# Optimization experiments

Measured on AMD Instinct MI355X. Metric: run time of the kernel, lower is better.

The kernel has to match this reference:

```python
import jax, jax.numpy as jnp
import numpy as np


def setup_inputs() -> dict:
    key = jax.random.key(0)
    ks = jax.random.split(key, 8)
    B, IN, H, OUT = 8192, 1024, 2048, 1024
    SIGMA_MIN, SIGMA_MAX, PHASE = 0.9, 0.999, 2.0 * np.pi
    # recurrence decay params, initialized as in the torch module
    rng = np.random.RandomState(0)
    u1 = rng.random_sample(H)
    u2 = rng.random_sample(H)
    v = -0.5 * np.log(u1 * (SIGMA_MAX ** 2 - SIGMA_MIN ** 2) + SIGMA_MIN ** 2)
    theta = u2 * PHASE
    scale_b = 1.0 / np.sqrt(IN)
    scale_c = 1.0 / np.sqrt(H)
    return {
        "x": jax.random.normal(ks[0], (B, IN), dtype=jnp.float32),
        "h_prev": jax.random.normal(ks[1], (B, H), dtype=jnp.float32),
        "Br": jax.random.normal(ks[2], (H, IN), dtype=jnp.float32) * scale_b,
        "Bi": jax.random.normal(ks[3], (H, IN), dtype=jnp.float32) * scale_b,
        "Cr": jax.random.normal(ks[4], (OUT, H), dtype=jnp.float32) * scale_c,
        "Ci": jax.random.normal(ks[5], (OUT, H), dtype=jnp.float32) * scale_c,
        "v_log": jnp.asarray(np.log(v), dtype=jnp.float32),
        "theta_log": jnp.asarray(np.log(theta), dtype=jnp.float32),
    }


def reference(x, h_prev, Br, Bi, Cr, Ci, v_log, theta_log):
    # effective diagonal recurrence weight w = exp(-exp(v_log) + i*exp(theta_log))
    mag = jnp.exp(-jnp.exp(v_log))            # [H]
    ang = jnp.exp(theta_log)                  # [H]
    wr = mag * jnp.cos(ang)
    wi = mag * jnp.sin(ang)
    # h = B(x) + h_prev * w  (h_prev is real -> imag part comes only from wi)
    # complexLinear on real x: real = x@Br^T, imag = x@Bi^T
    hr = jnp.einsum('bi,hi->bh', x, Br) + h_prev * wr   # [B,H]
    hi = jnp.einsum('bi,hi->bh', x, Bi) + h_prev * wi   # [B,H]
    # out = Re(C(h)) = hr@Cr^T - hi@Ci^T
    out = jnp.einsum('bh,oh->bo', hr, Cr) - jnp.einsum('bh,oh->bo', hi, Ci)
    return out
```

## Files before the change

kernel.cpp:

```cpp
#include <hip/hip_runtime.h>
#include <stdint.h>

typedef unsigned short u16;
typedef short bf16x8 __attribute__((ext_vector_type(8)));
typedef float f32x4 __attribute__((ext_vector_type(4)));

typedef void as1_void __attribute__((address_space(1)));
typedef void as3_void __attribute__((address_space(3)));

__device__ inline u16 f32_to_bf16(float f) {
    uint32_t u = __builtin_bit_cast(uint32_t, f);
    u += 0x7fffu + ((u >> 16) & 1u);
    return (u16)(u >> 16);
}

__device__ inline void gld_lds16(const void* g, void* l) {
    __builtin_amdgcn_global_load_lds((as1_void*)g, (as3_void*)l, 16, 0, 0);
}



__global__ void prep_kernel(const float* __restrict__ Cr, const float* __restrict__ Ci,
                            const float* __restrict__ Br, const float* __restrict__ Bi,
                            const float* __restrict__ v_log, const float* __restrict__ th_log,
                            u16* __restrict__ Ccat, u16* __restrict__ Bcat,
                            u16* __restrict__ Cwbf)
{
    __shared__ float t[32][33];
    const int b = blockIdx.x, tid = threadIdx.x;

    if (b < 2048) {
        int i = b * 256 + tid;
        int e = i * 4;
        int o = e >> 11;
        int h = e & 2047;
        float4 cr = *(const float4*)(Cr + (size_t)o * 2048 + h);
        float4 ci = *(const float4*)(Ci + (size_t)o * 2048 + h);
        ushort4 ucr, uci, ucw;
        ucr.x = f32_to_bf16(cr.x); ucr.y = f32_to_bf16(cr.y);
        ucr.z = f32_to_bf16(cr.z); ucr.w = f32_to_bf16(cr.w);
        uci.x = f32_to_bf16(-ci.x); uci.y = f32_to_bf16(-ci.y);
        uci.z = f32_to_bf16(-ci.z); uci.w = f32_to_bf16(-ci.w);
        float4 vl = *(const float4*)(v_log + h);
        float4 tl = *(const float4*)(th_log + h);
        float mag, ang, wr, wi;
        mag = expf(-expf(vl.x)); ang = expf(tl.x); wr = mag * cosf(ang); wi = mag * sinf(ang);
        ucw.x = f32_to_bf16(cr.x * wr - ci.x * wi);
        mag = expf(-expf(vl.y)); ang = expf(tl.y); wr = mag * cosf(ang); wi = mag * sinf(ang);
        ucw.y = f32_to_bf16(cr.y * wr - ci.y * wi);
        mag = expf(-expf(vl.z)); ang = expf(tl.z); wr = mag * cosf(ang); wi = mag * sinf(ang);
        ucw.z = f32_to_bf16(cr.z * wr - ci.z * wi);
        mag = expf(-expf(vl.w)); ang = expf(tl.w); wr = mag * cosf(ang); wi = mag * sinf(ang);
        ucw.w = f32_to_bf16(cr.w * wr - ci.w * wi);
        *(ushort4*)(Ccat + (size_t)o * 4096 + h)        = ucr;
        *(ushort4*)(Ccat + (size_t)o * 4096 + 2048 + h) = uci;
        *(ushort4*)(Cwbf + (size_t)o * 2048 + h)        = ucw;
    } else {
        int b2 = b - 2048;
        const float* src = (b2 & 2048) ? Bi : Br;
        int colOff = (b2 & 2048) ? 2048 : 0;
        int c0 = (b2 & 31) * 32, r0 = ((b2 >> 5) & 63) * 32;
        int tx = tid & 31, ty = tid >> 5;
#pragma unroll
        for (int j = 0; j < 4; j++)
            t[ty + j * 8][tx] = src[(size_t)(r0 + ty + j * 8) * 1024 + c0 + tx];
        __syncthreads();
#pragma unroll
        for (int j = 0; j < 4; j++)
            Bcat[(size_t)(c0 + ty + j * 8) * 4096 + colOff + r0 + tx] =
                f32_to_bf16(t[tx][ty + j * 8]);
    }
}


__global__ __launch_bounds__(256)
void gemm_splitk_kernel(const u16* __restrict__ A, const u16* __restrict__ B,
                        float* __restrict__ partials)
{
    __shared__ __align__(16) u16 ldsA[128 * 64];
    __shared__ __align__(16) u16 ldsB[128 * 64];
    const int K = 4096;

    const int tid = threadIdx.x, wid = tid >> 6, lane = tid & 63;
    const int quad = lane >> 4, l16 = lane & 15;
    const int wm = wid >> 1, wn = wid & 1;
    const int bm = blockIdx.y, bn = blockIdx.x, bz = blockIdx.z;
    const int kb = bz * 1024;

    const u16* gA[4]; const u16* gB[4];
    u16 *lA[4], *lB[4];
#pragma unroll
    for (int t = 0; t < 4; t++) {
        int s = wid * 256 + t * 64 + lane;
        int sr = s >> 3;
        int sj = (s & 7) ^ (sr & 7);
        lA[t] = ldsA + s * 8;
        lB[t] = ldsB + s * 8;
        gA[t] = A + (size_t)(bm * 128 + sr) * K + sj * 8 + kb;
        gB[t] = B + (size_t)(bn * 128 + sr) * K + sj * 8 + kb;
    }

    const f32x4 fz = {0.f, 0.f, 0.f, 0.f};
    f32x4 acc[4][4];
#pragma unroll
    for (int i = 0; i < 4; i++)
#pragma unroll
        for (int j = 0; j < 4; j++) acc[i][j] = fz;

    for (int k0 = 0; k0 < 1024; k0 += 64) {
        __syncthreads();
#pragma unroll
        for (int t = 0; t < 4; t++) {
            gld_lds16(gA[t] + k0, lA[t]);
            gld_lds16(gB[t] + k0, lB[t]);
        }
        __syncthreads();
#pragma unroll
        for (int ks = 0; ks < 2; ks++) {
            bf16x8 af[4], bfr[4];
#pragma unroll
            for (int i = 0; i < 4; i++) {
                int r = wm * 64 + i * 16 + l16;
                af[i] = *(const bf16x8*)(ldsA + (r * 8 + ((ks * 4 + quad) ^ (r & 7))) * 8);
            }
#pragma unroll
            for (int j = 0; j < 4; j++) {
                int r = wn * 64 + j * 16 + l16;
                bfr[j] = *(const bf16x8*)(ldsB + (r * 8 + ((ks * 4 + quad) ^ (r & 7))) * 8);
            }
#pragma unroll
            for (int i = 0; i < 4; i++)
#pragma unroll
                for (int j = 0; j < 4; j++)
                    acc[i][j] = __builtin_amdgcn_mfma_f32_16x16x32_bf16(af[i], bfr[j], acc[i][j], 0, 0, 0);
        }
    }

    float* P = partials + ((size_t)bz << 20);
    const int gm = bm * 128 + wm * 64, gn = bn * 128 + wn * 64;
#pragma unroll
    for (int i = 0; i < 4; i++)
#pragma unroll
        for (int j = 0; j < 4; j++) {
            int col = gn + j * 16 + l16;
#pragma unroll
            for (int r = 0; r < 4; r++)
                P[(size_t)(gm + i * 16 + quad * 4 + r) * 1024 + col] = acc[i][j][r];
        }
}


__global__ void reduce_cast_kernel(const float* __restrict__ partials,
                                   const float* __restrict__ x,
                                   const float* __restrict__ h_prev,
                                   u16* __restrict__ Wmain,
                                   u16* __restrict__ x_bf,
                                   u16* __restrict__ hp_bf)
{
    const int b = blockIdx.x, tid = threadIdx.x;
    if (b < 1024) {
        int i = b * 256 + tid;
        int e = i * 4;
        float4 s = *(const float4*)(partials + e);
#pragma unroll
        for (int z = 1; z < 4; z++) {
            float4 p = *(const float4*)(partials + ((size_t)z << 20) + e);
            s.x += p.x; s.y += p.y; s.z += p.z; s.w += p.w;
        }
        ushort4 u;
        u.x = f32_to_bf16(s.x); u.y = f32_to_bf16(s.y);
        u.z = f32_to_bf16(s.z); u.w = f32_to_bf16(s.w);
        ((ushort4*)Wmain)[i] = u;
    } else if (b < 9216) {
        int i = (b - 1024) * 256 + tid;
        float4 f = ((const float4*)x)[i];
        ushort4 o;
        o.x = f32_to_bf16(f.x); o.y = f32_to_bf16(f.y);
        o.z = f32_to_bf16(f.z); o.w = f32_to_bf16(f.w);
        ((ushort4*)x_bf)[i] = o;
    } else {
        int i = (b - 9216) * 256 + tid;
        float4 f = ((const float4*)h_prev)[i];
        ushort4 o;
        o.x = f32_to_bf16(f.x); o.y = f32_to_bf16(f.y);
        o.z = f32_to_bf16(f.z); o.w = f32_to_bf16(f.w);
        ((ushort4*)hp_bf)[i] = o;
    }
}


__global__ void reduce_only_kernel(const float* __restrict__ partials,
                                   u16* __restrict__ Wmain) {
    int i = blockIdx.x * blockDim.x + threadIdx.x;
    int e = i * 4;
    float4 s = *(const float4*)(partials + e);
#pragma unroll
    for (int z = 1; z < 4; z++) {
        float4 p = *(const float4*)(partials + ((size_t)z << 20) + e);
        s.x += p.x; s.y += p.y; s.z += p.z; s.w += p.w;
    }
    ushort4 u;
    u.x = f32_to_bf16(s.x); u.y = f32_to_bf16(s.y);
    u.z = f32_to_bf16(s.z); u.w = f32_to_bf16(s.w);
    ((ushort4*)Wmain)[i] = u;
}

__global__ void cast_both_kernel(const float* __restrict__ x,
                                 const float* __restrict__ h_prev,
                                 u16* __restrict__ dst) {
    const int n4x = 8192 * 1024 / 4;
    int i = blockIdx.x * blockDim.x + threadIdx.x;
    float4 f = (i < n4x) ? ((const float4*)x)[i] : ((const float4*)h_prev)[i - n4x];
    ushort4 o;
    o.x = f32_to_bf16(f.x); o.y = f32_to_bf16(f.y);
    o.z = f32_to_bf16(f.z); o.w = f32_to_bf16(f.w);
    ((ushort4*)dst)[i] = o;
}


__global__ __launch_bounds__(512)
void gemm_main_kernel(const u16* __restrict__ Axb, const u16* __restrict__ Ahb,
                      const u16* __restrict__ Bw,  const u16* __restrict__ Bcw,
                      float* __restrict__ out)
{
    __shared__ __align__(16) u16 lds[3][24576];

    const int tid = threadIdx.x, wid = tid >> 6, lane = tid & 63;
    const int quad = lane >> 4, l16 = lane & 15;
    const int wm = wid >> 1, wn = wid & 1;
    const int id = blockIdx.x;
    const int bm = id & 31, bn = id >> 5;

    int srA[4], sjA[4], srB[2], sjB[2];
#pragma unroll
    for (int q = 0; q < 4; q++) {
        int s = q * 512 + tid;
        srA[q] = s >> 3;
        sjA[q] = (s & 7) ^ (srA[q] & 7);
    }
#pragma unroll
    for (int q = 0; q < 2; q++) {
        int s = q * 512 + tid;
        srB[q] = s >> 3;
        sjB[q] = (s & 7) ^ (srB[q] & 7);
    }

    u16* buf0 = &lds[0][0];
    u16* buf1 = &lds[1][0];
    u16* buf2 = &lds[2][0];

    const f32x4 fz = {0.f, 0.f, 0.f, 0.f};
    f32x4 acc[4][4];
#pragma unroll
    for (int i = 0; i < 4; i++)
#pragma unroll
        for (int j = 0; j < 4; j++) acc[i][j] = fz;

    auto stage = [&](int tt, u16* buf) {
        const u16* Ab; const u16* Bb; int KS, koff;
        if (tt < 16) { Ab = Axb; Bb = Bw;  KS = 1024; koff = tt * 64; }
        else         { Ab = Ahb; Bb = Bcw; KS = 2048; koff = (tt - 16) * 64; }
#pragma unroll
        for (int q = 0; q < 4; q++)
            gld_lds16(Ab + (size_t)(bm * 256 + srA[q]) * KS + koff + sjA[q] * 8,
                      buf + (q * 512 + tid) * 8);
#pragma unroll
        for (int q = 0; q < 2; q++)
            gld_lds16(Bb + (size_t)(bn * 128 + srB[q]) * KS + koff + sjB[q] * 8,
                      buf + 16384 + (q * 512 + tid) * 8);
    };

    auto compute = [&](const u16* buf) {
#pragma unroll
        for (int ks = 0; ks < 2; ks++) {
            bf16x8 af[4], bfr[4];
#pragma unroll
            for (int i = 0; i < 4; i++) {
                int r = wm * 64 + i * 16 + l16;
                af[i] = *(const bf16x8*)(buf + (r * 8 + ((ks * 4 + quad) ^ (r & 7))) * 8);
            }
#pragma unroll
            for (int j = 0; j < 4; j++) {
                int r = wn * 64 + j * 16 + l16;
                bfr[j] = *(const bf16x8*)(buf + 16384 + (r * 8 + ((ks * 4 + quad) ^ (r & 7))) * 8);
            }
            __builtin_amdgcn_s_setprio(1);
#pragma unroll
            for (int i = 0; i < 4; i++)
#pragma unroll
                for (int j = 0; j < 4; j++)
                    acc[i][j] = __builtin_amdgcn_mfma_f32_16x16x32_bf16(af[i], bfr[j], acc[i][j], 0, 0, 0);
            __builtin_amdgcn_s_setprio(0);
        }
    };

#define PUBLISH(N)                                          \
    asm volatile("s_waitcnt vmcnt(" #N ")" ::: "memory");   \
    __builtin_amdgcn_s_barrier();                           \
    asm volatile("" ::: "memory")

    stage(0, buf0);
    stage(1, buf1);
    PUBLISH(6);

#pragma unroll 1
    for (int it = 0; it < 15; it++) {
        stage(3 * it + 2, buf2); compute(buf0); PUBLISH(6);
        stage(3 * it + 3, buf0); compute(buf1); PUBLISH(6);
        stage(3 * it + 4, buf1); compute(buf2); PUBLISH(6);
    }
    stage(47, buf2); compute(buf0); PUBLISH(6);
    compute(buf1); PUBLISH(0);
    compute(buf2);
#undef PUBLISH

    const int gm = bm * 256 + wm * 64, gn = bn * 128 + wn * 64;
#pragma unroll
    for (int i = 0; i < 4; i++)
#pragma unroll
        for (int j = 0; j < 4; j++) {
            int col = gn + j * 16 + l16;
#pragma unroll
            for (int r = 0; r < 4; r++)
                out[(size_t)(gm + i * 16 + quad * 4 + r) * 1024 + col] = acc[i][j][r];
        }
}


extern "C" void kernel_launch(void* const* d_in, const int* in_sizes, int n_in,
                              void* d_out, int out_size, void* d_ws, size_t ws_size,
                              hipStream_t stream)
{
    const float* x      = (const float*)d_in[0];
    const float* h_prev = (const float*)d_in[1];
    const float* Br     = (const float*)d_in[2];
    const float* Bi     = (const float*)d_in[3];
    const float* Cr     = (const float*)d_in[4];
    const float* Ci     = (const float*)d_in[5];
    const float* v_log  = (const float*)d_in[6];
    const float* th_log = (const float*)d_in[7];
    float* out = (float*)d_out;

    const size_t MB = 1024 * 1024;
    if (ws_size < 54 * MB) return;
    const bool big = (ws_size >= 86 * MB);

    char* ws = (char*)d_ws;
    u16*   Ccat     = (u16*)ws;
    u16*   Bcat     = (u16*)(ws + 8 * MB);
    float* partials = (float*)(ws + 16 * MB);
    u16*   x_bf     = (u16*)ws;
    u16*   Wmain    = (u16*)(ws + 48 * MB);
    u16*   Cwbf     = (u16*)(ws + 50 * MB);
    u16*   hp_bf    = big ? (u16*)(ws + 54 * MB) : (u16*)(ws + 16 * MB);

    prep_kernel<<<6144, 256, 0, stream>>>(Cr, Ci, Br, Bi, v_log, th_log,
                                          Ccat, Bcat, Cwbf);
    gemm_splitk_kernel<<<dim3(8, 8, 4), 256, 0, stream>>>(Ccat, Bcat, partials);
    if (big) {
        reduce_cast_kernel<<<25600, 256, 0, stream>>>(partials, x, h_prev,
                                                      Wmain, x_bf, hp_bf);
    } else {
        reduce_only_kernel<<<1024, 256, 0, stream>>>(partials, Wmain);
        cast_both_kernel<<<24576, 256, 0, stream>>>(x, h_prev, x_bf);
    }
    gemm_main_kernel<<<256, 512, 0, stream>>>(x_bf, hp_bf, Wmain, Cwbf, out);
}
```

Baseline: 242.2 us.

## Triple-buffer LDS in split-K GEMM to overlap global loads with MFMA

Replaces the single-buffered load-sync-compute loop with a three-stage LDS ring where tile k+2 is fetched via global_load_lds while tile k is computed. Barriers now wait only on vmcnt for the older stage. This hides global memory latency behind MFMA work. It also raises MFMA wave priority with s_setprio. LDS use rises to 96KB per block, which may lower occupancy.

```diff
diff --git a/kernel.cpp b/kernel.cpp
--- a/kernel.cpp
+++ b/kernel.cpp
@@ -77,8 +77,7 @@
 void gemm_splitk_kernel(const u16* __restrict__ A, const u16* __restrict__ B,
                         float* __restrict__ partials)
 {
-    __shared__ __align__(16) u16 ldsA[128 * 64];
-    __shared__ __align__(16) u16 ldsB[128 * 64];
+    __shared__ __align__(16) u16 lds[3][16384];
     const int K = 4096;
 
     const int tid = threadIdx.x, wid = tid >> 6, lane = tid & 63;
@@ -87,18 +86,17 @@
     const int bm = blockIdx.y, bn = blockIdx.x, bz = blockIdx.z;
     const int kb = bz * 1024;
 
-    const u16* gA[4]; const u16* gB[4];
-    u16 *lA[4], *lB[4];
-#pragma unroll
-    for (int t = 0; t < 4; t++) {
-        int s = wid * 256 + t * 64 + lane;
-        int sr = s >> 3;
-        int sj = (s & 7) ^ (sr & 7);
-        lA[t] = ldsA + s * 8;
-        lB[t] = ldsB + s * 8;
-        gA[t] = A + (size_t)(bm * 128 + sr) * K + sj * 8 + kb;
-        gB[t] = B + (size_t)(bn * 128 + sr) * K + sj * 8 + kb;
-    }
+    int sr[4], sj[4];
+#pragma unroll
+    for (int q = 0; q < 4; q++) {
+        int s = q * 256 + tid;
+        sr[q] = s >> 3;
+        sj[q] = (s & 7) ^ (sr[q] & 7);
+    }
+
+    u16* buf0 = &lds[0][0];
+    u16* buf1 = &lds[1][0];
+    u16* buf2 = &lds[2][0];
 
     const f32x4 fz = {0.f, 0.f, 0.f, 0.f};
     f32x4 acc[4][4];
@@ -107,34 +105,61 @@
 #pragma unroll
         for (int j = 0; j < 4; j++) acc[i][j] = fz;
 
-    for (int k0 = 0; k0 < 1024; k0 += 64) {
-        __syncthreads();
-#pragma unroll
-        for (int t = 0; t < 4; t++) {
-            gld_lds16(gA[t] + k0, lA[t]);
-            gld_lds16(gB[t] + k0, lB[t]);
-        }
-        __syncthreads();
+    auto stage = [&](int tt, u16* buf) {
+        int koff = kb + tt * 64;
+#pragma unroll
+        for (int q = 0; q < 4; q++) {
+            gld_lds16(A + (size_t)(bm * 128 + sr[q]) * K + koff + sj[q] * 8,
+                      buf + (q * 256 + tid) * 8);
+            gld_lds16(B + (size_t)(bn * 128 + sr[q]) * K + koff + sj[q] * 8,
+                      buf + 8192 + (q * 256 + tid) * 8);
+        }
+    };
+
+    auto compute = [&](const u16* buf) {
 #pragma unroll
         for (int ks = 0; ks < 2; ks++) {
             bf16x8 af[4], bfr[4];
 #pragma unroll
             for (int i = 0; i < 4; i++) {
                 int r = wm * 64 + i * 16 + l16;
-                af[i] = *(const bf16x8*)(ldsA + (r * 8 + ((ks * 4 + quad) ^ (r & 7))) * 8);
+                af[i] = *(const bf16x8*)(buf + (r * 8 + ((ks * 4 + quad) ^ (r & 7))) * 8);
             }
 #pragma unroll
             for (int j = 0; j < 4; j++) {
                 int r = wn * 64 + j * 16 + l16;
-                bfr[j] = *(const bf16x8*)(ldsB + (r * 8 + ((ks * 4 + quad) ^ (r & 7))) * 8);
+                bfr[j] = *(const bf16x8*)(buf + 8192 + (r * 8 + ((ks * 4 + quad) ^ (r & 7))) * 8);
             }
+            __builtin_amdgcn_s_setprio(1);
 #pragma unroll
             for (int i = 0; i < 4; i++)
 #pragma unroll
                 for (int j = 0; j < 4; j++)
                     acc[i][j] = __builtin_amdgcn_mfma_f32_16x16x32_bf16(af[i], bfr[j], acc[i][j], 0, 0, 0);
-        }
-    }
+            __builtin_amdgcn_s_setprio(0);
+        }
+    };
+
+#define PUBLISH(N)                                          \
+    asm volatile("s_waitcnt vmcnt(" #N ")" ::: "memory");   \
+    __builtin_amdgcn_s_barrier();                           \
+    asm volatile("" ::: "memory")
+
+    stage(0, buf0);
+    stage(1, buf1);
+    PUBLISH(8);
+
+#pragma unroll 1
+    for (int it = 0; it < 4; it++) {
+        stage(3 * it + 2, buf2); compute(buf0); PUBLISH(8);
+        stage(3 * it + 3, buf0); compute(buf1); PUBLISH(8);
+        stage(3 * it + 4, buf1); compute(buf2); PUBLISH(8);
+    }
+    stage(14, buf2); compute(buf0); PUBLISH(8);
+    stage(15, buf0); compute(buf1); PUBLISH(8);
+    compute(buf2); PUBLISH(0);
+    compute(buf0);
+#undef PUBLISH
 
     float* P = partials + ((size_t)bz << 20);
     const int gm = bm * 128 + wm * 64, gn = bn * 128 + wn * 64;
```

Result: no change. 239.4 us (-1.2%).
